# Kernel tuning notes

Measured on AMD Instinct MI355X. Metric: run time of the kernel, lower is better.

## Reference

```python
import jax, jax.numpy as jnp
import numpy as np

N = 65536      # total nodes (cells) in batch
E = 262144     # edges per edge type
T = 3          # edge types: row, col, diag
D = 128        # hidden_dim
HG = 4         # gat_heads
DHG = D // HG  # 32, GAT head dim
HH = 4         # hgt_heads
DHH = D // HH  # 32, HGT head dim
B = 32         # boards per batch
SLOPE = 0.2
EPS = 1e-6


def setup_inputs():
    ks = jax.random.split(jax.random.key(0), 32)
    def nrm(i, shape, s=0.05):
        return (jax.random.normal(ks[i], shape) * s).astype(jnp.float32)
    inp = {
        'x_cell': nrm(0, (N, D), 1.0),
        'z_h': nrm(1, (B, D), 1.0),
        'x_cell_embedded': nrm(2, (N, D), 1.0),
        'edge_index': jax.random.randint(ks[3], (T, 2, E), 0, N, dtype=jnp.int32),
        'batch_size': B,
        # GAT conv 1 (one GATConv per edge type, summed)
        'gat1_W': nrm(4, (T, D, D), 0.09),
        'gat1_asrc': nrm(5, (T, HG, DHG), 0.12),
        'gat1_adst': nrm(6, (T, HG, DHG), 0.12),
        'gat1_b': jnp.zeros((T, D), jnp.float32),
        # GAT conv 2
        'gat2_W': nrm(7, (T, D, D), 0.09),
        'gat2_asrc': nrm(8, (T, HG, DHG), 0.12),
        'gat2_adst': nrm(9, (T, HG, DHG), 0.12),
        'gat2_b': jnp.zeros((T, D), jnp.float32),
        # RMSNorms
        'norm1_s': jnp.ones((D,), jnp.float32),
        'norm2_s': jnp.ones((D,), jnp.float32),
        'norm3_s': jnp.ones((D,), jnp.float32),
        # HGT (single node type 'cell', T edge types)
        'hgt_Wk': nrm(10, (D, D), 0.09), 'hgt_bk': jnp.zeros((D,), jnp.float32),
        'hgt_Wq': nrm(11, (D, D), 0.09), 'hgt_bq': jnp.zeros((D,), jnp.float32),
        'hgt_Wv': nrm(12, (D, D), 0.09), 'hgt_bv': jnp.zeros((D,), jnp.float32),
        'hgt_arel': nrm(13, (T, HH, DHH, DHH), 0.15),
        'hgt_mrel': nrm(14, (T, HH, DHH, DHH), 0.15),
        'hgt_prel': jnp.ones((T, HH), jnp.float32),
        'hgt_Wo': nrm(15, (D, D), 0.09), 'hgt_bo': jnp.zeros((D,), jnp.float32),
        'hgt_skip': jnp.ones((), jnp.float32),
        # input injection
        'inj_W': nrm(16, (D, D), 0.09), 'inj_b': jnp.zeros((D,), jnp.float32),
        # FiLM
        'film_W1': nrm(17, (D, 2 * D), 0.09), 'film_b1': jnp.zeros((2 * D,), jnp.float32),
        'film_W2': nrm(18, (2 * D, 2 * D), 0.001), 'film_b2': jnp.zeros((2 * D,), jnp.float32),
    }
    return inp


def _rmsnorm(x, scale):
    return scale * x * jax.lax.rsqrt(jnp.mean(x * x, axis=-1, keepdims=True) + EPS)


def _res(x_old, x_new, scale):
    return jax.nn.leaky_relu(x_old + _rmsnorm(x_new, scale), SLOPE)


def _gat_sum(x, W, asrc, adst, b, src, dst):
    """HeteroConv(sum) over T GATConvs (concat heads, add_self_loops)."""
    loop = jnp.arange(N, dtype=src.dtype)
    def one(Wt, a_s, a_d, bt, s, t):
        s = jnp.concatenate([s, loop])   # self loops
        t = jnp.concatenate([t, loop])
        h = (x @ Wt).reshape(N, HG, DHG)             # [N,H,Dh]
        alpha_src = (h * a_s).sum(-1)                # [N,H]
        alpha_dst = (h * a_d).sum(-1)
        e = jax.nn.leaky_relu(alpha_src[s] + alpha_dst[t], SLOPE)  # [E+N,H]
        m = jax.ops.segment_max(e, t, num_segments=N)
        ex = jnp.exp(e - m[t])
        denom = jax.ops.segment_sum(ex, t, num_segments=N)
        alpha = ex / (denom[t] + 1e-16)
        out = jax.ops.segment_sum(alpha[:, :, None] * h[s], t, num_segments=N)
        return out.reshape(N, D) + bt
    return jax.vmap(one)(W, asrc, adst, b, src, dst).sum(0)


def _hgt(x, Wk, bk, Wq, bq, Wv, bv, a_rel, m_rel, p_rel, Wo, bo, skip, src, dst):
    k = (x @ Wk + bk).reshape(N, HH, DHH)
    q = (x @ Wq + bq).reshape(N, HH, DHH)
    v = (x @ Wv + bv).reshape(N, HH, DHH)
    # per-edge-type relation transforms at node level, then gather per edge
    k_t = jnp.einsum('nhd,thdf->tnhf', k, a_rel)    # [T,N,H,Dk]
    v_t = jnp.einsum('nhd,thdf->tnhf', v, m_rel)
    k_e = jax.vmap(lambda a, i: a[i])(k_t, src)     # [T,E,H,Dk]
    v_e = jax.vmap(lambda a, i: a[i])(v_t, src)
    score = (q[dst] * k_e).sum(-1) * p_rel[:, None, :] / np.sqrt(DHH)  # [T,E,H]
    score = score.reshape(T * E, HH)
    dst_f = dst.reshape(-1)
    m = jax.ops.segment_max(score, dst_f, num_segments=N)
    ex = jnp.exp(score - m[dst_f])
    denom = jax.ops.segment_sum(ex, dst_f, num_segments=N)
    alpha = ex / (denom[dst_f] + 1e-16)
    agg = jax.ops.segment_sum(alpha[:, :, None] * v_e.reshape(T * E, HH, DHH),
                              dst_f, num_segments=N)          # [N,H,Dk]
    out = jax.nn.gelu(agg.reshape(N, D), approximate=False) @ Wo + bo
    sig = jax.nn.sigmoid(skip)
    return sig * out + (1.0 - sig) * x


def _film(nodes, z_h, W1, b1, W2, b2, bsz):
    gb = jax.nn.gelu(z_h @ W1 + b1, approximate=False) @ W2 + b2  # [B,2D]
    gamma, beta = jnp.split(gb, 2, axis=-1)
    gamma = 0.1 * jnp.tanh(gamma)
    beta = 0.1 * jnp.tanh(beta)
    c = N // bsz
    out = (1.0 + gamma)[:, None, :] * nodes.reshape(bsz, c, D) + beta[:, None, :]
    return out.reshape(N, D)


def reference(x_cell, z_h, x_cell_embedded,
              gat1_W, gat1_asrc, gat1_adst, gat1_b,
              gat2_W, gat2_asrc, gat2_adst, gat2_b,
              norm1_s, norm2_s, norm3_s,
              hgt_Wk, hgt_bk, hgt_Wq, hgt_bq, hgt_Wv, hgt_bv,
              hgt_arel, hgt_mrel, hgt_prel, hgt_Wo, hgt_bo, hgt_skip,
              inj_W, inj_b, film_W1, film_b1, film_W2, film_b2,
              edge_index, batch_size):
    src = edge_index[:, 0]
    dst = edge_index[:, 1]
    x1 = _res(x_cell, _gat_sum(x_cell, gat1_W, gat1_asrc, gat1_adst, gat1_b, src, dst), norm1_s)
    x2 = _res(x1, _gat_sum(x1, gat2_W, gat2_asrc, gat2_adst, gat2_b, src, dst), norm2_s)
    x3 = _res(x2, _hgt(x2, hgt_Wk, hgt_bk, hgt_Wq, hgt_bq, hgt_Wv, hgt_bv,
                       hgt_arel, hgt_mrel, hgt_prel, hgt_Wo, hgt_bo, hgt_skip,
                       src, dst), norm3_s)
    x3 = x3 + x_cell_embedded @ inj_W + inj_b
    return _film(x3, z_h, film_W1, film_b1, film_W2, film_b2, batch_size)
```

## Files before the change

### kernel.cpp

```cpp
#include <hip/hip_runtime.h>

#define NN 65536
#define EE 262144
#define ND ((size_t)NN * 128)
#define TBW 132
#define WLP 136
#define NTOT (EE + NN)
#define CSRN (3*EE + 3*NN)

typedef unsigned short u16;
typedef short bf8_t __attribute__((ext_vector_type(8)));
typedef float f32x4 __attribute__((ext_vector_type(4)));

__device__ __forceinline__ float lrelu(float x){ return x > 0.f ? x : 0.2f*x; }
__device__ __forceinline__ float gelu_exact(float x){ return 0.5f*x*(1.f+erff(x*0.70710678118654752f)); }
__device__ __forceinline__ float fexp(float x){ return __expf(x); }
__device__ __forceinline__ u16 f2bf(float f){
    union { float f; unsigned u; } v; v.f = f;
    unsigned u = v.u;
    return (u16)((u + 0x7FFFu + ((u >> 16) & 1u)) >> 16);
}
__device__ __forceinline__ float bf2f(u16 b){
    union { unsigned u; float f; } v; v.u = ((unsigned)b) << 16; return v.f;
}
__device__ __forceinline__ float2 bf2x(unsigned p){
    union { unsigned u; float f; } a, b;
    a.u = (p & 0xFFFFu) << 16; b.u = p & 0xFFFF0000u;
    return make_float2(a.f, b.f);
}
__device__ __forceinline__ unsigned cvt2(float a, float b){
    unsigned r; asm("v_cvt_pk_bf16_f32 %0, %1, %2" : "=v"(r) : "v"(a), "v"(b)); return r;
}

__device__ __forceinline__ void load_af32(const float* __restrict__ X, int row, int lk, bf8_t* af){
    #pragma unroll
    for (int kk = 0; kk < 4; ++kk){
        const float* p = X + (size_t)row*128 + kk*32 + lk*8;
        float4 a = *(const float4*)p;
        float4 b = *(const float4*)(p+4);
        union { bf8_t v; unsigned u[4]; } r;
        r.u[0] = cvt2(a.x, a.y); r.u[1] = cvt2(a.z, a.w);
        r.u[2] = cvt2(b.x, b.y); r.u[3] = cvt2(b.z, b.w);
        af[kk] = r.v;
    }
}
__device__ __forceinline__ void load_af16(const u16* __restrict__ X, int row, int lk, bf8_t* af){
    #pragma unroll
    for (int kk = 0; kk < 4; ++kk)
        af[kk] = *(const bf8_t*)(X + (size_t)row*128 + kk*32 + lk*8);
}

__device__ __forceinline__ void stage_w(const u16* __restrict__ src, u16* __restrict__ wl, int tid){
    #pragma unroll
    for (int j = 0; j < 8; ++j){
        int o = (j*256 + tid)*8;
        bf8_t v = *(const bf8_t*)(src + o);
        *(bf8_t*)(wl + ((o>>7)*WLP + (o&127))) = v;
    }
}

__device__ __forceinline__ void mfma_l1_acc(const bf8_t* af, const u16* __restrict__ wl,
                                            int lr, int lk, f32x4* acc){
    #pragma unroll
    for (int kk = 0; kk < 4; ++kk){
        bf8_t B[8];
        #pragma unroll
        for (int nt = 0; nt < 8; ++nt)
            B[nt] = *(const bf8_t*)&wl[(nt*16+lr)*WLP + kk*32 + lk*8];
        #pragma unroll
        for (int nt = 0; nt < 8; ++nt)
            acc[nt] = __builtin_amdgcn_mfma_f32_16x16x32_bf16(af[kk], B[nt], acc[nt], 0, 0, 0);
    }
}
__device__ __forceinline__ void mfma_l1(const bf8_t* af, const u16* __restrict__ wl,
                                        int lr, int lk, f32x4* acc){
    #pragma unroll
    for (int i = 0; i < 8; ++i) acc[i] = (f32x4){0.f,0.f,0.f,0.f};
    mfma_l1_acc(af, wl, lr, lk, acc);
}
__device__ __forceinline__ void mfma_l2(const bf8_t* af0, const bf8_t* af1,
                                        const u16* __restrict__ wl,
                                        int lr, int lk, f32x4* acc0, f32x4* acc1){
    #pragma unroll
    for (int i = 0; i < 8; ++i){ acc0[i] = (f32x4){0.f,0.f,0.f,0.f}; acc1[i] = (f32x4){0.f,0.f,0.f,0.f}; }
    #pragma unroll
    for (int kk = 0; kk < 4; ++kk){
        bf8_t B[8];
        #pragma unroll
        for (int nt = 0; nt < 8; ++nt)
            B[nt] = *(const bf8_t*)&wl[(nt*16+lr)*WLP + kk*32 + lk*8];
        #pragma unroll
        for (int nt = 0; nt < 8; ++nt){
            acc0[nt] = __builtin_amdgcn_mfma_f32_16x16x32_bf16(af0[kk], B[nt], acc0[nt], 0, 0, 0);
            acc1[nt] = __builtin_amdgcn_mfma_f32_16x16x32_bf16(af1[kk], B[nt], acc1[nt], 0, 0, 0);
        }
    }
}

__device__ __forceinline__ void acc_to_tb(u16 (*tbw)[TBW], const f32x4* acc, int lr, int lk, const float* bias){
    asm volatile("s_waitcnt lgkmcnt(0)" ::: "memory");
    #pragma unroll
    for (int nt = 0; nt < 8; ++nt){
        int col = nt*16 + lr;
        float badd = bias ? bias[col] : 0.f;
        #pragma unroll
        for (int i = 0; i < 4; ++i) tbw[lk*4+i][col] = f2bf(acc[nt][i] + badd);
    }
    asm volatile("s_waitcnt lgkmcnt(0)" ::: "memory");
}
__device__ __forceinline__ void acc_to_tb_gelu(u16 (*tbw)[TBW], const f32x4* acc, int lr, int lk){
    asm volatile("s_waitcnt lgkmcnt(0)" ::: "memory");
    #pragma unroll
    for (int nt = 0; nt < 8; ++nt){
        int col = nt*16 + lr;
        #pragma unroll
        for (int i = 0; i < 4; ++i) tbw[lk*4+i][col] = f2bf(gelu_exact(acc[nt][i]));
    }
    asm volatile("s_waitcnt lgkmcnt(0)" ::: "memory");
}
__device__ __forceinline__ void tb_store(const u16 (*tbw)[TBW], u16* __restrict__ O, size_t rowstride, int rowbase, int lr, int lk){
    #pragma unroll
    for (int c = 0; c < 4; ++c){
        bf8_t v = *(const bf8_t*)&tbw[c*4+lk][lr*8];
        *(bf8_t*)(O + (size_t)(rowbase + c*4 + lk)*rowstride + lr*8) = v;
    }
}
__device__ __forceinline__ void tb_frags(const u16 (*tbw)[TBW], int lr, int lk, bf8_t* ha){
    #pragma unroll
    for (int kk = 0; kk < 4; ++kk) ha[kk] = *(const bf8_t*)&tbw[lr][kk*32 + lk*8];
}
__device__ __forceinline__ void tb_rows(const u16 (*tbw)[TBW], int lr, int lk, bf8_t* rw){
    #pragma unroll
    for (int c = 0; c < 4; ++c) rw[c] = *(const bf8_t*)&tbw[c*4+lk][lr*8];
}

__global__ __launch_bounds__(256) void wpack_k(
    const float* __restrict__ g1W, const float* __restrict__ g2W,
    const float* __restrict__ Wk, const float* __restrict__ Wq, const float* __restrict__ Wv,
    const float* __restrict__ Wo, const float* __restrict__ injW,
    const float* __restrict__ arel, const float* __restrict__ mrel,
    const float* __restrict__ g1as, const float* __restrict__ g1ad,
    const float* __restrict__ g2as, const float* __restrict__ g2ad,
    u16* __restrict__ wp, u16* __restrict__ wpa)
{
    int b = blockIdx.x, tid = threadIdx.x;
    if (b < 17) {
        const float* src; int rel = 0;
        if (b < 3) src = g1W + b*16384;
        else if (b < 6) src = g2W + (b-3)*16384;
        else if (b == 6) src = Wk;
        else if (b == 7) src = Wq;
        else if (b == 8) src = Wv;
        else if (b == 9) src = Wo;
        else if (b == 10) src = injW;
        else if (b < 14) { src = arel + (b-11)*4096; rel = 2; }
        else { src = mrel + (b-14)*4096; rel = 1; }
        u16* dst = wp + (size_t)b*16384;
        for (int idx = tid; idx < 16384; idx += 256) {
            int n = idx >> 7, k = idx & 127;
            float v;
            if (rel == 1)      v = ((n>>5)==(k>>5)) ? src[(n>>5)*1024 + (k&31)*32 + (n&31)] : 0.f;
            else if (rel == 2) v = ((n>>5)==(k>>5)) ? src[(n>>5)*1024 + (n&31)*32 + (k&31)] : 0.f;
            else               v = src[k*128 + n];
            dst[idx] = f2bf(v);
        }
    } else {
        for (int idx = tid; idx < 6*2048; idx += 256) {
            int m = idx >> 11;
            int j = idx & 2047;
            int cg = j >> 7, k = j & 127;
            const float* as = (m < 3) ? g1as : g2as;
            const float* ad = (m < 3) ? g1ad : g2ad;
            int t = (m < 3) ? m : m - 3;
            float v = 0.f;
            if (cg < 4)      { if ((k>>5)==cg)   v = as[t*128 + cg*32 + (k&31)]; }
            else if (cg < 8) { int g = cg-4; if ((k>>5)==g) v = ad[t*128 + g*32 + (k&31)]; }
            wpa[idx] = f2bf(v);
        }
    }
}

template<int AF32>
__global__ __launch_bounds__(256, 3) void gat_gemm3_k(const float* __restrict__ Xf, const u16* __restrict__ Xb,
    const u16* __restrict__ wpg, const u16* __restrict__ wpa,
    u16* __restrict__ hb, float* __restrict__ alsb, float* __restrict__ aldb)
{
    __shared__ __align__(16) u16 wl[128*WLP];
    __shared__ __align__(16) u16 tb[4][16][TBW];
    const int tid = threadIdx.x, wave = tid>>6, lane = tid&63, lr = lane&15, lk = lane>>4;
    const int t = blockIdx.y;
    const int rw0 = blockIdx.x*128 + wave*32;
    bf8_t af0[4], af1[4];
    if (AF32){ load_af32(Xf, rw0 + lr, lk, af0); load_af32(Xf, rw0 + 16 + lr, lk, af1); }
    else     { load_af16(Xb, rw0 + lr, lk, af0); load_af16(Xb, rw0 + 16 + lr, lk, af1); }
    stage_w(wpg + t*16384, wl, tid);
    bf8_t Ba[4];
    #pragma unroll
    for (int kk = 0; kk < 4; ++kk)
        Ba[kk] = *(const bf8_t*)&wpa[t*2048 + lr*128 + kk*32 + lk*8];
    __syncthreads();
    f32x4 acc0[8], acc1[8];
    mfma_l2(af0, af1, wl, lr, lk, acc0, acc1);
    u16* h = hb + (size_t)t*ND;
    float* alst = alsb + (size_t)t*NN*4;
    float* aldt = aldb + (size_t)t*NN*4;
    {
        acc_to_tb(tb[wave], acc0, lr, lk, nullptr);
        tb_store(tb[wave], h, 128, rw0, lr, lk);
        bf8_t ha[4]; tb_frags(tb[wave], lr, lk, ha);
        f32x4 a2 = (f32x4){0.f,0.f,0.f,0.f};
        #pragma unroll
        for (int kk = 0; kk < 4; ++kk)
            a2 = __builtin_amdgcn_mfma_f32_16x16x32_bf16(ha[kk], Ba[kk], a2, 0, 0, 0);
        if (lr < 8){
            float* dp = (lr < 4) ? alst : aldt;
            int g = lr & 3;
            #pragma unroll
            for (int i = 0; i < 4; ++i) dp[(size_t)(rw0 + lk*4 + i)*4 + g] = a2[i];
        }
    }
    {
        acc_to_tb(tb[wave], acc1, lr, lk, nullptr);
        tb_store(tb[wave], h, 128, rw0 + 16, lr, lk);
        bf8_t ha[4]; tb_frags(tb[wave], lr, lk, ha);
        f32x4 a2 = (f32x4){0.f,0.f,0.f,0.f};
        #pragma unroll
        for (int kk = 0; kk < 4; ++kk)
            a2 = __builtin_amdgcn_mfma_f32_16x16x32_bf16(ha[kk], Ba[kk], a2, 0, 0, 0);
        if (lr < 8){
            float* dp = (lr < 4) ? alst : aldt;
            int g = lr & 3;
            #pragma unroll
            for (int i = 0; i < 4; ++i) dp[(size_t)(rw0 + 16 + lk*4 + i)*4 + g] = a2[i];
        }
    }
}

__global__ __launch_bounds__(256, 3) void hgt_proj_k(const u16* __restrict__ X,
    const u16* __restrict__ wpk, const u16* __restrict__ wpq, const u16* __restrict__ wpv,
    const u16* __restrict__ wparel,
    const float* __restrict__ bk, const float* __restrict__ bq, const float* __restrict__ bv,
    u16* __restrict__ kvb, u16* __restrict__ qtb)
{
    __shared__ __align__(16) u16 wl[128*WLP];
    __shared__ __align__(16) u16 tb[4][16][TBW];
    const int tid = threadIdx.x, wave = tid>>6, lane = tid&63, lr = lane&15, lk = lane>>4;
    const int task = blockIdx.y;
    const int rw0 = blockIdx.x*128 + wave*32;
    bf8_t af0[4], af1[4];
    load_af16(X, rw0 + lr, lk, af0);
    load_af16(X, rw0 + 16 + lr, lk, af1);
    f32x4 acc0[8], acc1[8];
    if (task == 0) {
        stage_w(wpk, wl, tid);
        __syncthreads();
        mfma_l2(af0, af1, wl, lr, lk, acc0, acc1);
        acc_to_tb(tb[wave], acc0, lr, lk, bk); tb_store(tb[wave], kvb, 256, rw0, lr, lk);
        acc_to_tb(tb[wave], acc1, lr, lk, bk); tb_store(tb[wave], kvb, 256, rw0 + 16, lr, lk);
    } else if (task == 1) {
        stage_w(wpv, wl, tid);
        __syncthreads();
        mfma_l2(af0, af1, wl, lr, lk, acc0, acc1);
        acc_to_tb(tb[wave], acc0, lr, lk, bv); tb_store(tb[wave], kvb + 128, 256, rw0, lr, lk);
        acc_to_tb(tb[wave], acc1, lr, lk, bv); tb_store(tb[wave], kvb + 128, 256, rw0 + 16, lr, lk);
    } else {
        const int t = task - 2;
        stage_w(wpq, wl, tid);
        __syncthreads();
        mfma_l2(af0, af1, wl, lr, lk, acc0, acc1);
        bf8_t ha0[4], ha1[4];
        acc_to_tb(tb[wave], acc0, lr, lk, bq); tb_frags(tb[wave], lr, lk, ha0);
        acc_to_tb(tb[wave], acc1, lr, lk, bq); tb_frags(tb[wave], lr, lk, ha1);
        __syncthreads();
        stage_w(wparel + t*16384, wl, tid);
        __syncthreads();
        mfma_l2(ha0, ha1, wl, lr, lk, acc0, acc1);
        u16* o = qtb + (size_t)t*ND;
        acc_to_tb(tb[wave], acc0, lr, lk, nullptr); tb_store(tb[wave], o, 128, rw0, lr, lk);
        acc_to_tb(tb[wave], acc1, lr, lk, nullptr); tb_store(tb[wave], o, 128, rw0 + 16, lr, lk);
    }
}

__global__ __launch_bounds__(256) void hist_k(const int* __restrict__ ei, int* __restrict__ cnt){
    int gid = blockIdx.x*256 + threadIdx.x;
    int t = gid / EE, e = gid - t*EE;
    int d = ei[t*2*EE + EE + e];
    atomicAdd(&cnt[t*NN + d], 1);
}
__global__ __launch_bounds__(256) void scanA_k(const int* __restrict__ cnt, int* __restrict__ s0off, int* __restrict__ parts){
    __shared__ int sums[256];
    int b = blockIdx.x; int base = b * 1024;
    int tid = threadIdx.x;
    int v[4]; int tsum = 0;
    #pragma unroll
    for (int i = 0; i < 4; ++i){
        int n = base + tid*4 + i;
        v[i] = cnt[n] + cnt[NN+n] + cnt[2*NN+n] + 3;
        tsum += v[i];
    }
    sums[tid] = tsum; __syncthreads();
    for (int ofs = 1; ofs < 256; ofs <<= 1) {
        int a = (tid >= ofs) ? sums[tid-ofs] : 0;
        __syncthreads();
        sums[tid] += a;
        __syncthreads();
    }
    int run = sums[tid] - tsum;
    #pragma unroll
    for (int i = 0; i < 4; ++i){ s0off[base + tid*4 + i] = run; run += v[i]; }
    if (tid == 255) parts[b] = sums[255];
}
__global__ void scan2_k(int* parts){
    if (threadIdx.x == 0 && blockIdx.x == 0) {
        int run = 0;
        for (int i = 0; i < 64; ++i) { int v = parts[i]; parts[i] = run; run += v; }
    }
}
__global__ __launch_bounds__(256) void scanB_k(const int* __restrict__ cnt, int* __restrict__ s0off,
                                               int* __restrict__ s1off, int* __restrict__ s2off,
                                               const int* __restrict__ parts){
    int b = blockIdx.x; int base = b * 1024;
    int add = parts[b];
    #pragma unroll
    for (int i = 0; i < 4; ++i){
        int n = base + threadIdx.x*4 + i;
        int m = s0off[n] + add;
        int c0 = cnt[n], c1 = cnt[NN+n];
        s0off[n] = m;
        s1off[n] = m + c0 + 1;
        s2off[n] = m + c0 + c1 + 2;
    }
    if (b == 0 && threadIdx.x == 0) s0off[NN] = CSRN;
}
__global__ __launch_bounds__(256) void selffill_k(const int* __restrict__ s0off, const int* __restrict__ s1off,
                                                  const int* __restrict__ s2off, int* __restrict__ csrc){
    int gid = blockIdx.x*256 + threadIdx.x;
    int t = gid / NN, n = gid - t*NN;
    int pos = (t==0) ? s0off[n] : (t==1 ? s1off[n] : s2off[n]);
    csrc[pos] = n;
}
__global__ __launch_bounds__(256) void scatter_k(const int* __restrict__ ei,
    const int* __restrict__ s0off, const int* __restrict__ s1off, const int* __restrict__ s2off,
    int* __restrict__ cur, int* __restrict__ csrc, int* __restrict__ posmap){
    int gid = blockIdx.x*256 + threadIdx.x;
    int t = gid / EE, e = gid - t*EE;
    int s = ei[t*2*EE + e];
    int d = ei[t*2*EE + EE + e];
    int p = atomicAdd(&cur[t*NN + d], 1);
    int basep = (t==0) ? s0off[d] : (t==1 ? s1off[d] : s2off[d]);
    int pos = basep + 1 + p;
    csrc[pos] = s;
    posmap[t*EE + e] = pos;
}

__global__ __launch_bounds__(256) void alpha_k(const float* __restrict__ alsb, const float* __restrict__ aldb,
    const int* __restrict__ ei, const int* __restrict__ posmap,
    const int* __restrict__ s0off, const int* __restrict__ s1off, const int* __restrict__ s2off,
    float4* __restrict__ ab)
{
    int gid = blockIdx.x*256 + threadIdx.x;
    int t = gid / NTOT, r = gid - t*NTOT;
    int s, d, pos;
    if (r < EE) {
        s = ei[t*2*EE + r];
        d = ei[t*2*EE + EE + r];
        pos = posmap[t*EE + r];
    } else {
        int n = r - EE;
        s = n; d = n;
        pos = (t==0) ? s0off[n] : (t==1 ? s1off[n] : s2off[n]);
    }
    const float* As = alsb + ((size_t)t*NN + s)*4;
    const float* Ad = aldb + ((size_t)t*NN + d)*4;
    float4 o;
    o.x = fexp(lrelu(As[0] + Ad[0]));
    o.y = fexp(lrelu(As[1] + Ad[1]));
    o.z = fexp(lrelu(As[2] + Ad[2]));
    o.w = fexp(lrelu(As[3] + Ad[3]));
    ab[pos] = o;
}

template<int XF32>
__global__ __launch_bounds__(256) void gat_aggres_k(const u16* __restrict__ hb,
    const float* __restrict__ abf,
    const int* __restrict__ s0off, const int* __restrict__ s1off, const int* __restrict__ s2off,
    const int* __restrict__ csrc,
    const float* __restrict__ bias3, const float* __restrict__ xoldf, const u16* __restrict__ xoldb,
    const float* __restrict__ scale, u16* __restrict__ outb)
{
    int gid = blockIdx.x*256 + threadIdx.x;
    int node = gid >> 6, lane = gid & 63;
    int eh = lane >> 5, hh = (lane >> 3) & 3, cp = lane & 7;
    int ch = hh*32 + cp*4;
    int segb[4] = { s0off[node], s1off[node], s2off[node], s0off[node+1] };
    float a[4] = {0.f, 0.f, 0.f, 0.f};
    #pragma unroll
    for (int t = 0; t < 3; ++t) {
        const u16* h = hb + (size_t)t*ND;
        int beg = segb[t], end = segb[t+1];
        float ds = 0.f, s0 = 0.f, s1 = 0.f, s2 = 0.f, s3 = 0.f;
        for (int pos = beg; pos < end; pos += 4) {
            int p0 = pos + eh, p1 = pos + 2 + eh;
            int v0 = (p0 < end), v1 = (p1 < end);
            int q0 = v0 ? p0 : beg, q1 = v1 ? p1 : beg;
            int sA = csrc[q0], sB = csrc[q1];
            float alA = abf[(size_t)q0*4 + hh];
            float alB = abf[(size_t)q1*4 + hh];
            uint2 hA = *(const uint2*)&h[(size_t)sA*128 + ch];
            uint2 hB = *(const uint2*)&h[(size_t)sB*128 + ch];
            alA = v0 ? alA : 0.f;
            alB = v1 ? alB : 0.f;
            float2 wA0 = bf2x(hA.x), wA1 = bf2x(hA.y);
            float2 wB0 = bf2x(hB.x), wB1 = bf2x(hB.y);
            ds += alA + alB;
            s0 += alA*wA0.x + alB*wB0.x;
            s1 += alA*wA0.y + alB*wB0.y;
            s2 += alA*wA1.x + alB*wB1.x;
            s3 += alA*wA1.y + alB*wB1.y;
        }
        ds += __shfl_xor(ds, 32);
        s0 += __shfl_xor(s0, 32);
        s1 += __shfl_xor(s1, 32);
        s2 += __shfl_xor(s2, 32);
        s3 += __shfl_xor(s3, 32);
        float inv = 1.f/(ds + 1e-16f);
        a[0] += s0*inv; a[1] += s1*inv; a[2] += s2*inv; a[3] += s3*inv;
    }
    float4 b0 = *(const float4*)&bias3[ch];
    float4 b1 = *(const float4*)&bias3[128 + ch];
    float4 b2 = *(const float4*)&bias3[256 + ch];
    a[0] += b0.x + b1.x + b2.x;
    a[1] += b0.y + b1.y + b2.y;
    a[2] += b0.z + b1.z + b2.z;
    a[3] += b0.w + b1.w + b2.w;
    float ssum = a[0]*a[0] + a[1]*a[1] + a[2]*a[2] + a[3]*a[3];
    ssum += __shfl_xor(ssum, 1); ssum += __shfl_xor(ssum, 2);
    ssum += __shfl_xor(ssum, 4); ssum += __shfl_xor(ssum, 8);
    ssum += __shfl_xor(ssum, 16);
    float r = rsqrtf(ssum*(1.f/128.f) + 1e-6f);
    float4 sc = *(const float4*)&scale[ch];
    size_t off = (size_t)node*128 + ch;
    float x0, x1v, x2v, x3;
    if (XF32) {
        float4 xo = *(const float4*)&xoldf[off];
        x0 = xo.x; x1v = xo.y; x2v = xo.z; x3 = xo.w;
    } else {
        uint2 xo = *(const uint2*)&xoldb[off];
        float2 p0 = bf2x(xo.x), p1 = bf2x(xo.y);
        x0 = p0.x; x1v = p0.y; x2v = p1.x; x3 = p1.y;
    }
    float y0 = lrelu(x0  + sc.x*a[0]*r);
    float y1 = lrelu(x1v + sc.y*a[1]*r);
    float y2 = lrelu(x2v + sc.z*a[2]*r);
    float y3 = lrelu(x3  + sc.w*a[3]*r);
    uint2 o2; o2.x = cvt2(y0, y1); o2.y = cvt2(y2, y3);
    *(uint2*)&outb[off] = o2;
}

__global__ __launch_bounds__(256) void hgt_agg_k(const u16* __restrict__ kvb,
    const u16* __restrict__ qtb, const float* __restrict__ prel,
    const int* __restrict__ s0off, const int* __restrict__ s1off, const int* __restrict__ s2off,
    const int* __restrict__ csrc, u16* __restrict__ pb)
{
    int gid = blockIdx.x*256 + threadIdx.x;
    int node = gid >> 6, lane = gid & 63;
    int eh = lane >> 5, hh = (lane >> 3) & 3, cp = lane & 7;
    int ch = hh*32 + cp*4;
    const float S = 0.17677669529663689f;
    int segb[4] = { s0off[node], s1off[node], s2off[node], s0off[node+1] };
    float dsum = 0.f;
    float ac[3][4];
    #pragma unroll
    for (int t = 0; t < 3; ++t){ ac[t][0]=0.f; ac[t][1]=0.f; ac[t][2]=0.f; ac[t][3]=0.f; }
    #pragma unroll
    for (int t = 0; t < 3; ++t) {
        float ph = prel[t*4 + hh] * S;
        uint2 qw = *(const uint2*)&qtb[(size_t)t*ND + (size_t)node*128 + ch];
        float2 q0 = bf2x(qw.x), q1 = bf2x(qw.y);
        int self = segb[t];
        int beg = self + 1, end = segb[t+1];
        for (int pos = beg; pos < end; pos += 4) {
            int p0 = pos + eh, p1 = pos + 2 + eh;
            int v0 = (p0 < end), v1 = (p1 < end);
            int qp0 = v0 ? p0 : self, qp1 = v1 ? p1 : self;
            int sA = csrc[qp0], sB = csrc[qp1];
            size_t rA = (size_t)sA*256 + ch, rB = (size_t)sB*256 + ch;
            uint2 kA = *(const uint2*)&kvb[rA], kB = *(const uint2*)&kvb[rB];
            uint2 vA = *(const uint2*)&kvb[rA + 128], vB = *(const uint2*)&kvb[rB + 128];
            float2 kA0 = bf2x(kA.x), kA1 = bf2x(kA.y);
            float2 kB0 = bf2x(kB.x), kB1 = bf2x(kB.y);
            float scA = kA0.x*q0.x + kA0.y*q0.y + kA1.x*q1.x + kA1.y*q1.y;
            float scB = kB0.x*q0.x + kB0.y*q0.y + kB1.x*q1.x + kB1.y*q1.y;
            scA += __shfl_xor(scA, 1); scB += __shfl_xor(scB, 1);
            scA += __shfl_xor(scA, 2); scB += __shfl_xor(scB, 2);
            scA += __shfl_xor(scA, 4); scB += __shfl_xor(scB, 4);
            float eA = v0 ? fexp(scA*ph) : 0.f;
            float eB = v1 ? fexp(scB*ph) : 0.f;
            float2 vA0 = bf2x(vA.x), vA1 = bf2x(vA.y);
            float2 vB0 = bf2x(vB.x), vB1 = bf2x(vB.y);
            dsum += eA + eB;
            ac[t][0] += eA*vA0.x + eB*vB0.x;
            ac[t][1] += eA*vA0.y + eB*vB0.y;
            ac[t][2] += eA*vA1.x + eB*vB1.x;
            ac[t][3] += eA*vA1.y + eB*vB1.y;
        }
    }
    dsum += __shfl_xor(dsum, 32);
    #pragma unroll
    for (int t = 0; t < 3; ++t){
        ac[t][0] += __shfl_xor(ac[t][0], 32);
        ac[t][1] += __shfl_xor(ac[t][1], 32);
        ac[t][2] += __shfl_xor(ac[t][2], 32);
        ac[t][3] += __shfl_xor(ac[t][3], 32);
    }
    float inv = 1.f/(dsum + 1e-16f);
    size_t o = (size_t)node*128 + ch;
    #pragma unroll
    for (int t = 0; t < 3; ++t){
        uint2 o2;
        o2.x = cvt2(ac[t][0]*inv, ac[t][1]*inv);
        o2.y = cvt2(ac[t][2]*inv, ac[t][3]*inv);
        *(uint2*)&pb[(size_t)t*ND + o] = o2;
    }
}

__global__ __launch_bounds__(256, 3) void final_k(const u16* __restrict__ pb,
    const u16* __restrict__ wpmrel, const u16* __restrict__ wpo, const float* __restrict__ bo,
    const u16* __restrict__ x2b, const float* __restrict__ skipp, const float* __restrict__ scale,
    const float* __restrict__ xemb, const u16* __restrict__ wpinj, const float* __restrict__ injb,
    const float* __restrict__ gbuf, const int* __restrict__ bszp,
    float* __restrict__ out)
{
    __shared__ __align__(16) u16 wl[128*WLP];
    __shared__ __align__(16) u16 tb[4][16][TBW];
    const int tid = threadIdx.x, wave = tid>>6, lane = tid&63, lr = lane&15, lk = lane>>4;
    const int rw = blockIdx.x*64 + wave*16;
    f32x4 acc[8];
    #pragma unroll
    for (int i = 0; i < 8; ++i) acc[i] = (f32x4){0.f,0.f,0.f,0.f};
    for (int t = 0; t < 3; ++t){
        if (t) __syncthreads();
        bf8_t a0[4]; load_af16(pb + (size_t)t*ND, rw + lr, lk, a0);
        stage_w(wpmrel + t*16384, wl, tid);
        __syncthreads();
        mfma_l1_acc(a0, wl, lr, lk, acc);
    }
    bf8_t ga[4];
    acc_to_tb_gelu(tb[wave], acc, lr, lk);
    tb_frags(tb[wave], lr, lk, ga);
    __syncthreads();
    stage_w(wpo, wl, tid);
    __syncthreads();
    mfma_l1(ga, wl, lr, lk, acc);
    bf8_t hw[4];
    acc_to_tb(tb[wave], acc, lr, lk, bo);
    tb_rows(tb[wave], lr, lk, hw);
    bf8_t e0[4];
    load_af32(xemb, rw + lr, lk, e0);
    __syncthreads();
    stage_w(wpinj, wl, tid);
    __syncthreads();
    mfma_l1(e0, wl, lr, lk, acc);
    bf8_t in[4];
    acc_to_tb(tb[wave], acc, lr, lk, injb);
    tb_rows(tb[wave], lr, lk, in);
    const float sig = 1.f/(1.f + expf(-skipp[0]));
    const int cpb = NN / *bszp;
    float4 sca = *(const float4*)&scale[lr*8];
    float4 scb = *(const float4*)&scale[lr*8 + 4];
    #pragma unroll
    for (int c = 0; c < 4; ++c){
        int row = rw + c*4 + lk;
        bf8_t x8 = *(const bf8_t*)(x2b + (size_t)row*128 + lr*8);
        float x[8], v[8];
        float ssl = 0.f;
        #pragma unroll
        for (int j = 0; j < 8; ++j){
            x[j] = bf2f((u16)x8[j]);
            float h = bf2f((u16)hw[c][j]);
            v[j] = sig*h + (1.f - sig)*x[j];
            ssl += v[j]*v[j];
        }
        ssl += __shfl_xor(ssl, 1); ssl += __shfl_xor(ssl, 2);
        ssl += __shfl_xor(ssl, 4); ssl += __shfl_xor(ssl, 8);
        float rq = rsqrtf(ssl*(1.f/128.f) + 1e-6f);
        const float* gr = gbuf + (row / cpb)*256;
        float4 g0 = *(const float4*)&gr[lr*8];
        float4 g1 = *(const float4*)&gr[lr*8 + 4];
        float4 b0 = *(const float4*)&gr[128 + lr*8];
        float4 b1 = *(const float4*)&gr[128 + lr*8 + 4];
        float4 oA, oB;
        #pragma unroll
        for (int j = 0; j < 8; ++j){
            float scj = (j < 4) ? ((const float*)&sca)[j] : ((const float*)&scb)[j-4];
            float y = lrelu(x[j] + scj*v[j]*rq);
            float hf = y + bf2f((u16)in[c][j]);
            float gj = (j < 4) ? ((const float*)&g0)[j] : ((const float*)&g1)[j-4];
            float bj = (j < 4) ? ((const float*)&b0)[j] : ((const float*)&b1)[j-4];
            float ov = (1.f + gj)*hf + bj;
            if (j < 4) ((float*)&oA)[j] = ov; else ((float*)&oB)[j-4] = ov;
        }
        *(float4*)(out + (size_t)row*128 + lr*8)     = oA;
        *(float4*)(out + (size_t)row*128 + lr*8 + 4) = oB;
    }
}

__global__ __launch_bounds__(256) void film_k(const float* __restrict__ z,
    const float* __restrict__ W1, const float* __restrict__ b1,
    const float* __restrict__ W2, const float* __restrict__ b2,
    float* __restrict__ gb)
{
    __shared__ float zr[128];
    __shared__ float g1[256];
    int r = blockIdx.x, tid = threadIdx.x;
    if (tid < 128) zr[tid] = z[r*128 + tid];
    __syncthreads();
    float s = b1[tid];
    for (int k = 0; k < 128; ++k) s += zr[k]*W1[k*256 + tid];
    g1[tid] = gelu_exact(s);
    __syncthreads();
    float s2 = b2[tid];
    for (int k = 0; k < 256; ++k) s2 += g1[k]*W2[k*256 + tid];
    gb[r*256 + tid] = 0.1f*tanhf(s2);
}

extern "C" void kernel_launch(void* const* d_in, const int* in_sizes, int n_in,
                              void* d_out, int out_size, void* d_ws, size_t ws_size,
                              hipStream_t stream)
{
    const float* x_cell = (const float*)d_in[0];
    const float* z_h    = (const float*)d_in[1];
    const float* x_emb  = (const float*)d_in[2];
    const int*   eidx   = (const int*)d_in[3];
    const int*   bszp   = (const int*)d_in[4];
    const float* g1W  = (const float*)d_in[5];
    const float* g1as = (const float*)d_in[6];
    const float* g1ad = (const float*)d_in[7];
    const float* g1b  = (const float*)d_in[8];
    const float* g2W  = (const float*)d_in[9];
    const float* g2as = (const float*)d_in[10];
    const float* g2ad = (const float*)d_in[11];
    const float* g2b  = (const float*)d_in[12];
    const float* n1s  = (const float*)d_in[13];
    const float* n2s  = (const float*)d_in[14];
    const float* n3s  = (const float*)d_in[15];
    const float* Wk   = (const float*)d_in[16];
    const float* bk   = (const float*)d_in[17];
    const float* Wq   = (const float*)d_in[18];
    const float* bq   = (const float*)d_in[19];
    const float* Wv   = (const float*)d_in[20];
    const float* bv   = (const float*)d_in[21];
    const float* arel = (const float*)d_in[22];
    const float* mrel = (const float*)d_in[23];
    const float* prel = (const float*)d_in[24];
    const float* Wo   = (const float*)d_in[25];
    const float* bo   = (const float*)d_in[26];
    const float* skipp= (const float*)d_in[27];
    const float* injW = (const float*)d_in[28];
    const float* injb = (const float*)d_in[29];
    const float* fW1  = (const float*)d_in[30];
    const float* fb1  = (const float*)d_in[31];
    const float* fW2  = (const float*)d_in[32];
    const float* fb2  = (const float*)d_in[33];

    u16* wp   = (u16*)d_ws;
    u16* wpa  = wp + (size_t)17*16384;
    float4* ab = (float4*)(wpa + 6*2048);
    u16* x1b  = (u16*)(ab + CSRN);
    u16* x2b  = x1b + ND;
    u16* kvb  = x2b + ND;
    u16* pb   = kvb + 2*ND;
    u16* hb   = pb + 3*ND;
    float* alsb = (float*)(hb + 3*ND);
    float* aldb = alsb + (size_t)3*NN*4;
    float* gbuf = aldb + (size_t)3*NN*4;
    int* s0off  = (int*)(gbuf + 32*256);
    int* s1off  = s0off + (NN+1);
    int* s2off  = s1off + NN;
    int* csrc   = s2off + NN;
    int* posmap = csrc + CSRN;
    int* tmpc   = posmap + 3*EE;
    int* cur    = tmpc + 3*NN;
    int* parts  = cur + 3*NN;

    u16* qtb = hb;
    float* outp = (float*)d_out;

    const u16* wpg1 = wp;
    const u16* wpg2 = wp + (size_t)3*16384;
    const u16* wpk  = wp + (size_t)6*16384;
    const u16* wpq  = wp + (size_t)7*16384;
    const u16* wpv  = wp + (size_t)8*16384;
    const u16* wpo  = wp + (size_t)9*16384;
    const u16* wpinj= wp + (size_t)10*16384;
    const u16* wparel = wp + (size_t)11*16384;
    const u16* wpmrel = wp + (size_t)14*16384;

    wpack_k<<<18, 256, 0, stream>>>(g1W, g2W, Wk, Wq, Wv, Wo, injW, arel, mrel,
                                    g1as, g1ad, g2as, g2ad, wp, wpa);

    hipMemsetAsync(tmpc, 0, 3*NN*sizeof(int), stream);
    hist_k<<<3*EE/256, 256, 0, stream>>>(eidx, tmpc);
    scanA_k<<<64, 256, 0, stream>>>(tmpc, s0off, parts);
    scan2_k<<<1, 64, 0, stream>>>(parts);
    scanB_k<<<64, 256, 0, stream>>>(tmpc, s0off, s1off, s2off, parts);
    selffill_k<<<3*NN/256, 256, 0, stream>>>(s0off, s1off, s2off, csrc);
    hipMemsetAsync(cur, 0, 3*NN*sizeof(int), stream);
    scatter_k<<<3*EE/256, 256, 0, stream>>>(eidx, s0off, s1off, s2off, cur, csrc, posmap);

    int B = in_sizes[1] / 128;
    film_k<<<B, 256, 0, stream>>>(z_h, fW1, fb1, fW2, fb2, gbuf);

    gat_gemm3_k<1><<<dim3(512,3), 256, 0, stream>>>(x_cell, nullptr, wpg1, wpa, hb, alsb, aldb);
    alpha_k<<<3*NTOT/256, 256, 0, stream>>>(alsb, aldb, eidx, posmap, s0off, s1off, s2off, ab);
    gat_aggres_k<1><<<16384, 256, 0, stream>>>(hb, (const float*)ab, s0off, s1off, s2off, csrc,
                                               g1b, x_cell, nullptr, n1s, x1b);

    gat_gemm3_k<0><<<dim3(512,3), 256, 0, stream>>>(nullptr, x1b, wpg2, wpa + 3*2048, hb, alsb, aldb);
    alpha_k<<<3*NTOT/256, 256, 0, stream>>>(alsb, aldb, eidx, posmap, s0off, s1off, s2off, ab);
    gat_aggres_k<0><<<16384, 256, 0, stream>>>(hb, (const float*)ab, s0off, s1off, s2off, csrc,
                                               g2b, nullptr, x1b, n2s, x2b);

    hgt_proj_k<<<dim3(512,5), 256, 0, stream>>>(x2b, wpk, wpq, wpv, wparel,
                                                bk, bq, bv, kvb, qtb);
    hgt_agg_k<<<16384, 256, 0, stream>>>(kvb, qtb, prel, s0off, s1off, s2off, csrc, pb);

    final_k<<<1024, 256, 0, stream>>>(pb, wpmrel, wpo, bo, x2b, skipp, n3s,
                                      x_emb, wpinj, injb, gbuf, bszp, outp);
}
```

Baseline: 588.9 us.

## Exploit block-diagonal HGT relation matrices with compact packing and direct global fragment loads

The per-head relation matrices (a_rel, m_rel) were previously packed as dense 128x128 block-diagonal bf16 matrices, staged through LDS and multiplied with full-K MFMA loops. They are now packed compactly in MFMA fragment order and loaded straight from global memory, one MFMA per output tile, using only the matching head's K slice. This removes three quarters of the MFMAs and all LDS staging and barriers for those stages in hgt_proj_k and final_k. final_k also now stages Wo and loads x_emb up front so those loads overlap the relation products. The cost is uncoalesced-ish global fragment reads that depend on cache hits.

```diff
diff --git a/kernel.cpp b/kernel.cpp
--- a/kernel.cpp
+++ b/kernel.cpp
@@ -96,6 +96,29 @@
         }
     }
 }
+__device__ __forceinline__ void mfma_bd1_acc(const bf8_t* af, const u16* __restrict__ Bp,
+                                             int lr, int lk, f32x4* acc){
+    bf8_t B[8];
+    #pragma unroll
+    for (int nt = 0; nt < 8; ++nt)
+        B[nt] = *(const bf8_t*)&Bp[nt*512 + lr*32 + lk*8];
+    #pragma unroll
+    for (int nt = 0; nt < 8; ++nt)
+        acc[nt] = __builtin_amdgcn_mfma_f32_16x16x32_bf16(af[nt>>1], B[nt], acc[nt], 0, 0, 0);
+}
+__device__ __forceinline__ void mfma_bd2(const bf8_t* af0, const bf8_t* af1,
+                                         const u16* __restrict__ Bp,
+                                         int lr, int lk, f32x4* acc0, f32x4* acc1){
+    bf8_t B[8];
+    #pragma unroll
+    for (int nt = 0; nt < 8; ++nt)
+        B[nt] = *(const bf8_t*)&Bp[nt*512 + lr*32 + lk*8];
+    #pragma unroll
+    for (int nt = 0; nt < 8; ++nt){
+        acc0[nt] = __builtin_amdgcn_mfma_f32_16x16x32_bf16(af0[nt>>1], B[nt], (f32x4){0.f,0.f,0.f,0.f}, 0, 0, 0);
+        acc1[nt] = __builtin_amdgcn_mfma_f32_16x16x32_bf16(af1[nt>>1], B[nt], (f32x4){0.f,0.f,0.f,0.f}, 0, 0, 0);
+    }
+}
 
 __device__ __forceinline__ void acc_to_tb(u16 (*tbw)[TBW], const f32x4* acc, int lr, int lk, const float* bias){
     asm volatile("s_waitcnt lgkmcnt(0)" ::: "memory");
@@ -144,24 +167,29 @@
     u16* __restrict__ wp, u16* __restrict__ wpa)
 {
     int b = blockIdx.x, tid = threadIdx.x;
-    if (b < 17) {
-        const float* src; int rel = 0;
+    if (b < 11) {
+        const float* src;
         if (b < 3) src = g1W + b*16384;
         else if (b < 6) src = g2W + (b-3)*16384;
         else if (b == 6) src = Wk;
         else if (b == 7) src = Wq;
         else if (b == 8) src = Wv;
         else if (b == 9) src = Wo;
-        else if (b == 10) src = injW;
-        else if (b < 14) { src = arel + (b-11)*4096; rel = 2; }
-        else { src = mrel + (b-14)*4096; rel = 1; }
+        else src = injW;
         u16* dst = wp + (size_t)b*16384;
         for (int idx = tid; idx < 16384; idx += 256) {
             int n = idx >> 7, k = idx & 127;
-            float v;
-            if (rel == 1)      v = ((n>>5)==(k>>5)) ? src[(n>>5)*1024 + (k&31)*32 + (n&31)] : 0.f;
-            else if (rel == 2) v = ((n>>5)==(k>>5)) ? src[(n>>5)*1024 + (n&31)*32 + (k&31)] : 0.f;
-            else               v = src[k*128 + n];
+            dst[idx] = f2bf(src[k*128 + n]);
+        }
+    } else if (b < 17) {
+        int rel2 = (b < 14);
+        const float* src = rel2 ? (arel + (b-11)*4096) : (mrel + (b-14)*4096);
+        u16* dst = wp + (size_t)11*16384 + (size_t)(b-11)*4096;
+        for (int idx = tid; idx < 4096; idx += 256) {
+            int nt = idx >> 9, rest = idx & 511;
+            int lr = rest >> 5, kp = rest & 31;
+            int h = nt >> 1, c = (nt & 1)*16 + lr;
+            float v = rel2 ? src[h*1024 + c*32 + kp] : src[h*1024 + kp*32 + c];
             dst[idx] = f2bf(v);
         }
     } else {
@@ -238,7 +266,7 @@
 
 __global__ __launch_bounds__(256, 3) void hgt_proj_k(const u16* __restrict__ X,
     const u16* __restrict__ wpk, const u16* __restrict__ wpq, const u16* __restrict__ wpv,
-    const u16* __restrict__ wparel,
+    const u16* __restrict__ wpad,
     const float* __restrict__ bk, const float* __restrict__ bq, const float* __restrict__ bv,
     u16* __restrict__ kvb, u16* __restrict__ qtb)
 {
@@ -271,10 +299,7 @@
         bf8_t ha0[4], ha1[4];
         acc_to_tb(tb[wave], acc0, lr, lk, bq); tb_frags(tb[wave], lr, lk, ha0);
         acc_to_tb(tb[wave], acc1, lr, lk, bq); tb_frags(tb[wave], lr, lk, ha1);
-        __syncthreads();
-        stage_w(wparel + t*16384, wl, tid);
-        __syncthreads();
-        mfma_l2(ha0, ha1, wl, lr, lk, acc0, acc1);
+        mfma_bd2(ha0, ha1, wpad + t*4096, lr, lk, acc0, acc1);
         u16* o = qtb + (size_t)t*ND;
         acc_to_tb(tb[wave], acc0, lr, lk, nullptr); tb_store(tb[wave], o, 128, rw0, lr, lk);
         acc_to_tb(tb[wave], acc1, lr, lk, nullptr); tb_store(tb[wave], o, 128, rw0 + 16, lr, lk);
@@ -525,7 +550,7 @@
 }
 
 __global__ __launch_bounds__(256, 3) void final_k(const u16* __restrict__ pb,
-    const u16* __restrict__ wpmrel, const u16* __restrict__ wpo, const float* __restrict__ bo,
+    const u16* __restrict__ wpmd, const u16* __restrict__ wpo, const float* __restrict__ bo,
     const u16* __restrict__ x2b, const float* __restrict__ skipp, const float* __restrict__ scale,
     const float* __restrict__ xemb, const u16* __restrict__ wpinj, const float* __restrict__ injb,
     const float* __restrict__ gbuf, const int* __restrict__ bszp,
@@ -535,28 +560,25 @@
     __shared__ __align__(16) u16 tb[4][16][TBW];
     const int tid = threadIdx.x, wave = tid>>6, lane = tid&63, lr = lane&15, lk = lane>>4;
     const int rw = blockIdx.x*64 + wave*16;
+    stage_w(wpo, wl, tid);
+    bf8_t e0[4];
+    load_af32(xemb, rw + lr, lk, e0);
     f32x4 acc[8];
     #pragma unroll
     for (int i = 0; i < 8; ++i) acc[i] = (f32x4){0.f,0.f,0.f,0.f};
+    #pragma unroll
     for (int t = 0; t < 3; ++t){
-        if (t) __syncthreads();
         bf8_t a0[4]; load_af16(pb + (size_t)t*ND, rw + lr, lk, a0);
-        stage_w(wpmrel + t*16384, wl, tid);
-        __syncthreads();
-        mfma_l1_acc(a0, wl, lr, lk, acc);
+        mfma_bd1_acc(a0, wpmd + t*4096, lr, lk, acc);
     }
     bf8_t ga[4];
     acc_to_tb_gelu(tb[wave], acc, lr, lk);
     tb_frags(tb[wave], lr, lk, ga);
-    __syncthreads();
-    stage_w(wpo, wl, tid);
     __syncthreads();
     mfma_l1(ga, wl, lr, lk, acc);
     bf8_t hw[4];
     acc_to_tb(tb[wave], acc, lr, lk, bo);
     tb_rows(tb[wave], lr, lk, hw);
-    bf8_t e0[4];
-    load_af32(xemb, rw + lr, lk, e0);
     __syncthreads();
     stage_w(wpinj, wl, tid);
     __syncthreads();
@@ -693,8 +715,8 @@
     const u16* wpv  = wp + (size_t)8*16384;
     const u16* wpo  = wp + (size_t)9*16384;
     const u16* wpinj= wp + (size_t)10*16384;
-    const u16* wparel = wp + (size_t)11*16384;
-    const u16* wpmrel = wp + (size_t)14*16384;
+    const u16* wpad = wp + (size_t)11*16384;
+    const u16* wpmd = wpad + (size_t)3*4096;
 
     wpack_k<<<18, 256, 0, stream>>>(g1W, g2W, Wk, Wq, Wv, Wo, injW, arel, mrel,
                                     g1as, g1ad, g2as, g2ad, wp, wpa);
@@ -721,10 +743,10 @@
     gat_aggres_k<0><<<16384, 256, 0, stream>>>(hb, (const float*)ab, s0off, s1off, s2off, csrc,
                                                g2b, nullptr, x1b, n2s, x2b);
 
-    hgt_proj_k<<<dim3(512,5), 256, 0, stream>>>(x2b, wpk, wpq, wpv, wparel,
+    hgt_proj_k<<<dim3(512,5), 256, 0, stream>>>(x2b, wpk, wpq, wpv, wpad,
                                                 bk, bq, bv, kvb, qtb);
     hgt_agg_k<<<16384, 256, 0, stream>>>(kvb, qtb, prel, s0off, s1off, s2off, csrc, pb);
 
-    final_k<<<1024, 256, 0, stream>>>(pb, wpmrel, wpo, bo, x2b, skipp, n3s,
+    final_k<<<1024, 256, 0, stream>>>(pb, wpmd, wpo, bo, x2b, skipp, n3s,
                                       x_emb, wpinj, injb, gbuf, bszp, outp);
 }
```

Result: faster. 562.9 us (-4.4%).
